# Kernel tuning notes

Measured on AMD Instinct MI355X. Metric: run time of the kernel, lower is better.

The kernel has to match this reference:

```python
import jax, jax.numpy as jnp
import numpy as np

BS, N, DX, DE, STEPS = 32, 64, 8, 5, 50


def setup_inputs() -> dict:
    key = jax.random.key(0)
    kx, ke, km, kg, kwx, kwe = jax.random.split(key, 6)
    # one-hot node states [bs, n, dx]
    x_lab = jax.random.randint(kx, (BS, N), 0, DX)
    X = jax.nn.one_hot(x_lab, DX, dtype=jnp.float32)
    # symmetric one-hot edge states [bs, n, n, de], zero diagonal
    e_lab = jax.random.randint(ke, (BS, N, N), 0, DE)
    e_lab = jnp.triu(e_lab, 1)
    e_lab = e_lab + jnp.swapaxes(e_lab, 1, 2)
    E = jax.nn.one_hot(e_lab, DE, dtype=jnp.float32)
    # variable-size graphs: first `length` nodes valid
    lengths = jax.random.randint(km, (BS,), N // 2, N + 1)
    node_mask = jnp.arange(N)[None, :] < lengths[:, None]
    gammas = jax.random.uniform(kg, (STEPS,), minval=1e-3, maxval=2e-2)
    # stub denoising network weights (stand-in for the graph transformer `net`)
    Wx = jax.random.normal(kwx, (DX, DX)) * 0.5
    We = jax.random.normal(kwe, (DE, DE)) * 0.5
    return {"X": X, "E": E, "node_mask": node_mask, "gammas": gammas, "Wx": Wx, "We": We}


def _langevin(X, E, gammas, Wx, We, node_mask):
    bs, n, dx = X.shape
    de = E.shape[-1]
    nm = node_mask.astype(X.dtype)                    # [bs, n]
    em = nm[:, :, None] * nm[:, None, :]              # [bs, n, n]
    em = em * (1.0 - jnp.eye(n, dtype=X.dtype))       # zero diagonal
    iu = jnp.triu(jnp.ones((n, n), dtype=bool), 1)    # strict upper triangle
    key0 = jax.random.key(42)

    def step(carry, inp):
        Xc, Ec = carry
        gamma, k = inp
        kx, ke = jax.random.split(jax.random.fold_in(key0, k))
        # --- stub `net` forward: per-class linear map + softmax ---
        predX = jax.nn.softmax(Xc @ Wx, axis=-1) * gamma          # pred.X * gamma
        predE = jax.nn.softmax(Ec @ We, axis=-1) * gamma          # pred.E * gamma
        predE = 0.5 * (predE + jnp.swapaxes(predE, 1, 2))         # symmetric edges
        # --- scatter_(argmax, 0); scatter_(argmax, clamp(1-sum,0)); normalize ---
        ohx = jax.nn.one_hot(jnp.argmax(Xc, -1), dx, dtype=Xc.dtype)
        ohe = jax.nn.one_hot(jnp.argmax(Ec, -1), de, dtype=Ec.dtype)
        predX = predX * (1.0 - ohx)
        predE = predE * (1.0 - ohe)
        predX = predX + ohx * jnp.maximum(1.0 - predX.sum(-1, keepdims=True), 0.0)
        predE = predE + ohe * jnp.maximum(1.0 - predE.sum(-1, keepdims=True), 0.0)
        predX = predX / predX.sum(-1, keepdims=True)
        predE = predE / predE.sum(-1, keepdims=True)
        # --- categorical sample (Gumbel-argmax), one-hot, symmetrize, mask ---
        sx = jnp.argmax(jnp.log(predX) + jax.random.gumbel(kx, predX.shape), -1)
        se = jnp.argmax(jnp.log(predE) + jax.random.gumbel(ke, predE.shape), -1)
        se = jnp.where(iu[None], se, 0)
        se = se + jnp.swapaxes(se, 1, 2)
        Xn = jax.nn.one_hot(sx, dx, dtype=Xc.dtype) * nm[:, :, None]
        En = jax.nn.one_hot(se, de, dtype=Ec.dtype) * em[..., None]
        return (Xn, En), (Xc, Ec, Xn, En)

    ks = jnp.arange(STEPS)
    _, (outX, outE, totX, totE) = jax.lax.scan(step, (X, E), (gammas, ks))
    tr = lambda a: jnp.moveaxis(a, 0, 1)             # [steps,bs,...] -> [bs,steps,...]
    return tr(totX), tr(totE), tr(outX), tr(outE)


def reference(X, E, node_mask, gammas, Wx, We):
    return _langevin(X, E, gammas, Wx, We, node_mask)
```

## Files before the change

### kernel.cpp

```cpp
#include <hip/hip_runtime.h>
#include <stdint.h>

#pragma clang fp contract(off)

#define STEPS 50
#define BSZ 32
#define NN 64
#define DXC 8
#define DEC 5
#define OFF_TOTE 819200UL
#define OFF_OUTX 33587200UL
#define OFF_OUTE 34406400UL

#define NPAIR 2016
#define EDGE_CHAINS 64512
#define NODE_CHAINS 2048
#define EBLK 16128
#define WS_KEYS 0UL
#define WS_CL   1024UL
#define WS_GE   130048UL
#define WS_GN   64642048UL
#define WS_S2E  67918848UL
#define WS_S2N  71144448UL
#define WS_NEED 71246848UL

__device__ __forceinline__ uint32_t rotl32(uint32_t x, int d) {
  return (x << d) | (x >> (32 - d));
}

__device__ __forceinline__ void tf2x32(uint32_t k0, uint32_t k1,
                                       uint32_t x0, uint32_t x1,
                                       uint32_t& o0, uint32_t& o1) {
  uint32_t ks2 = k0 ^ k1 ^ 0x1BD11BDAu;
  x0 += k0; x1 += k1;
#define TF_R(r) { x0 += x1; x1 = rotl32(x1, (r)); x1 ^= x0; }
  TF_R(13) TF_R(15) TF_R(26) TF_R(6)
  x0 += k1; x1 += ks2 + 1u;
  TF_R(17) TF_R(29) TF_R(16) TF_R(24)
  x0 += ks2; x1 += k0 + 2u;
  TF_R(13) TF_R(15) TF_R(26) TF_R(6)
  x0 += k0; x1 += k1 + 3u;
  TF_R(17) TF_R(29) TF_R(16) TF_R(24)
  x0 += k1; x1 += ks2 + 4u;
  TF_R(13) TF_R(15) TF_R(26) TF_R(6)
  x0 += ks2; x1 += k0 + 5u;
#undef TF_R
  o0 = x0; o1 = x1;
}

__device__ __forceinline__ float logf_cr(float x) { return (float)log((double)x); }
__device__ __forceinline__ float expf_cr(float x) { return (float)exp((double)x); }

__device__ __forceinline__ float gumbel_inl(uint32_t k0, uint32_t k1,
                                            uint32_t idx) {
  uint32_t o0, o1;
  tf2x32(k0, k1, 0u, idx, o0, o1);
  uint32_t bits = o0 ^ o1;
  float uf = __uint_as_float((bits >> 9) | 0x3f800000u) - 1.0f;
  float u = fmaxf(uf, 1.1754943508222875e-38f);
  return -logf_cr(-logf_cr(u));
}
__device__ __attribute__((noinline)) float gumbel_part(uint32_t k0, uint32_t k1,
                                                       uint32_t idx) {
  return gumbel_inl(k0, k1, idx);
}

__device__ __forceinline__ bool detect_bf16(const void* X) {
  const uint16_t* u = (const uint16_t*)X;
  int c = 0;
  for (int i = 0; i < 16; ++i) c += (u[i] == 0x3F80u);
  return c >= 2;
}

__device__ __forceinline__ float ld(const void* p, size_t i, bool bf) {
  if (bf) return __uint_as_float(((uint32_t)((const uint16_t*)p)[i]) << 16);
  return ((const float*)p)[i];
}
__device__ __forceinline__ void st(void* p, size_t i, bool bf, float v) {
  if (bf) ((uint16_t*)p)[i] = (uint16_t)(__float_as_uint(v) >> 16);
  else ((float*)p)[i] = v;
}
__device__ __forceinline__ void stv4(void* p, size_t e4, bool bf,
                                     float a, float b, float c, float d) {
  if (!bf) {
    float4 v; v.x = a; v.y = b; v.z = c; v.w = d;
    ((float4*)p)[e4] = v;
  } else {
    ushort4 v;
    v.x = (uint16_t)(__float_as_uint(a) >> 16);
    v.y = (uint16_t)(__float_as_uint(b) >> 16);
    v.z = (uint16_t)(__float_as_uint(c) >> 16);
    v.w = (uint16_t)(__float_as_uint(d) >> 16);
    ((ushort4*)p)[e4] = v;
  }
}
__device__ __forceinline__ void cpy4(void* dst, const void* src, size_t de4,
                                     size_t se4, bool bf) {
  if (!bf) ((float4*)dst)[de4] = ((const float4*)src)[se4];
  else ((uint2*)dst)[de4] = ((const uint2*)src)[se4];
}

__device__ __forceinline__ bool read_mask(const void* mp, int idx) {
  const uint8_t* m8 = (const uint8_t*)mp;
  uint8_t b1 = m8[1];
  if (b1 == 0) return ((const uint32_t*)mp)[idx] != 0;
  if (b1 == 0x3F) return ((const uint16_t*)mp)[idx] != 0;
  return m8[idx] != 0;
}

template <int D>
__device__ void fill_logp(const void* __restrict__ W, bool bf, float gamma,
                          int c, float* __restrict__ out) {
  float t[D];
  for (int d = 0; d < D; ++d) t[d] = ld(W, c * D + d, bf);
  float m = t[0];
  for (int d = 1; d < D; ++d) m = fmaxf(m, t[d]);
  float u[D];
  for (int d = 0; d < D; ++d) u[d] = expf_cr(t[d] - m);
  float s = 0.0f;
  for (int d = 0; d < D; ++d) s += u[d];
  float p[D];
  for (int d = 0; d < D; ++d) p[d] = (u[d] / s) * gamma;
  p[c] = 0.0f;
  float s1 = 0.0f;
  for (int d = 0; d < D; ++d) s1 += p[d];
  float r = fmaxf(1.0f - s1, 0.0f);
  p[c] = r;
  float s2 = 0.0f;
  for (int d = 0; d < D; ++d) s2 += p[d];
  for (int d = 0; d < D; ++d) out[d] = logf_cr(p[d] / s2);
}

__device__ __forceinline__ void pair_decode(int q, int& lo, int& hi) {
  lo = 0; int rem = q;
  while (rem >= 63 - lo) { rem -= 63 - lo; lo++; }
  hi = lo + 1 + rem;
}

__global__ void key_kernel(uint8_t* __restrict__ ws) {
  int t = threadIdx.x;
  uint32_t* wk = (uint32_t*)(ws + WS_KEYS);
  if (t == 0) wk[200] = 0u;
  if (t < STEPS) {
    uint32_t f0, f1, a0, a1;
    tf2x32(0u, 42u, 0u, (uint32_t)t, f0, f1);
    tf2x32(f0, f1, 0u, 0u, a0, a1);
    wk[2 * t] = a0; wk[2 * t + 1] = a1;
    tf2x32(f0, f1, 0u, 1u, a0, a1);
    wk[100 + 2 * t] = a0; wk[101 + 2 * t] = a1;
  }
}

__global__ __launch_bounds__(256) void compact_kernel(const void* __restrict__ M,
                                                      uint8_t* __restrict__ ws) {
  int chain = blockIdx.x * 256 + threadIdx.x;
  if (chain >= EDGE_CHAINS) return;
  int b = chain / NPAIR, q = chain % NPAIR, lo, hi;
  pair_decode(q, lo, hi);
  if (read_mask(M, b * NN + lo) && read_mask(M, b * NN + hi)) {
    uint32_t slot = atomicAdd((uint32_t*)(ws + WS_KEYS) + 200, 1u);
    ((uint16_t*)(ws + WS_CL))[slot] = (uint16_t)chain;
  }
}

__global__ __launch_bounds__(256) void gumbel_kernel(const void* __restrict__ M,
                                                     uint8_t* __restrict__ ws) {
  const uint32_t* keys = (const uint32_t*)(ws + WS_KEYS);
  float* ge = (float*)(ws + WS_GE);
  float* gn = (float*)(ws + WS_GN);
  int blk = blockIdx.x, tid = threadIdx.x;
  if (blk < EBLK) {
    uint32_t cnt = keys[200];
    if ((uint32_t)(blk * 4) >= cnt) return;
    if (tid >= STEPS * DEC) return;
    const uint16_t* cl = (const uint16_t*)(ws + WS_CL);
    int k = tid / DEC, d = tid % DEC;
    uint32_t kk0 = keys[100 + 2 * k], kk1 = keys[101 + 2 * k];
    int ch[4]; uint32_t ctr[4]; bool ok[4];
#pragma unroll
    for (int j = 0; j < 4; ++j) {
      uint32_t idx = (uint32_t)(blk * 4 + j);
      ok[j] = idx < cnt;
      int chain = cl[ok[j] ? idx : 0];
      ch[j] = chain;
      int b = chain / NPAIR, q = chain % NPAIR, lo, hi;
      pair_decode(q, lo, hi);
      ctr[j] = (uint32_t)(((b * NN + lo) * NN + hi) * DEC + d);
    }
    float v0 = gumbel_inl(kk0, kk1, ctr[0]);
    float v1 = gumbel_inl(kk0, kk1, ctr[1]);
    float v2 = gumbel_inl(kk0, kk1, ctr[2]);
    float v3 = gumbel_inl(kk0, kk1, ctr[3]);
    if (ok[0]) ge[(size_t)ch[0] * 250 + tid] = v0;
    if (ok[1]) ge[(size_t)ch[1] * 250 + tid] = v1;
    if (ok[2]) ge[(size_t)ch[2] * 250 + tid] = v2;
    if (ok[3]) ge[(size_t)ch[3] * 250 + tid] = v3;
  } else {
    int n0 = (blk - EBLK) * 4;
    bool ok[4];
#pragma unroll
    for (int j = 0; j < 4; ++j) ok[j] = read_mask(M, n0 + j);
    for (int r = 0; r < 2; ++r) {
      int slot = r * 256 + tid;
      if (slot < STEPS * DXC) {
        int k = slot >> 3, d = slot & 7;
        uint32_t kk0 = keys[2 * k], kk1 = keys[2 * k + 1];
        float w[4];
#pragma unroll
        for (int j = 0; j < 4; ++j)
          w[j] = gumbel_inl(kk0, kk1, (uint32_t)((n0 + j) * DXC + d));
#pragma unroll
        for (int j = 0; j < 4; ++j)
          if (ok[j]) gn[(size_t)(n0 + j) * 400 + slot] = w[j];
      }
    }
  }
}

__global__ __launch_bounds__(256) void chain_kernel(
    const void* __restrict__ X, const void* __restrict__ E,
    const void* __restrict__ M, const void* __restrict__ gammas,
    const void* __restrict__ Wx, const void* __restrict__ We,
    uint8_t* __restrict__ ws) {
  __shared__ float stab[STEPS * DXC * DXC];
  const bool edge_blk = blockIdx.x < 252;
  const int t = threadIdx.x;
  const bool bf = detect_bf16(X);

  if (edge_blk) {
    for (int task = t; task < STEPS * DEC; task += 256)
      fill_logp<DEC>(We, bf, ld(gammas, task / DEC, bf), task % DEC,
                     &stab[task * DEC]);
  } else {
    for (int task = t; task < STEPS * DXC; task += 256)
      fill_logp<DXC>(Wx, bf, ld(gammas, task / DXC, bf), task % DXC,
                     &stab[task * DXC]);
  }
  __syncthreads();

  if (edge_blk) {
    int chain = blockIdx.x * 256 + t;
    int b = chain / NPAIR, q = chain % NPAIR, lo, hi;
    pair_decode(q, lo, hi);
    if (!(read_mask(M, b * NN + lo) && read_mask(M, b * NN + hi))) return;
    size_t crow = (((size_t)(b * NN + lo)) * NN + hi) * DEC;
    int cur = 0;
    float bst = ld(E, crow, bf);
    for (int d = 1; d < DEC; ++d) {
      float v = ld(E, crow + d, bf);
      if (v > bst) { bst = v; cur = d; }
    }
    const float* g = (const float*)(ws + WS_GE) + (size_t)chain * 250;
    uint8_t* s2e = ws + WS_S2E;
    for (int k = 0; k < STEPS; ++k) {
      const float* le = stab + (k * DEC + cur) * DEC;
      const float* gk = g + k * DEC;
      float bs = -3.0e38f; int nxt = 0;
      for (int d = 0; d < DEC; ++d) {
        float s = le[d] + gk[d];
        if (s > bs) { bs = s; nxt = d; }
      }
      s2e[(size_t)(b * STEPS + k) * NPAIR + q] = (uint8_t)nxt;
      cur = nxt;
    }
  } else {
    int node = (int)(blockIdx.x - 252) * 256 + t;
    if (!read_mask(M, node)) return;
    int b = node >> 6, i = node & 63;
    int cur = 0;
    float bst = ld(X, (size_t)node * DXC, bf);
    for (int d = 1; d < DXC; ++d) {
      float v = ld(X, (size_t)node * DXC + d, bf);
      if (v > bst) { bst = v; cur = d; }
    }
    const float* g = (const float*)(ws + WS_GN) + (size_t)node * 400;
    uint8_t* s2n = ws + WS_S2N;
    for (int k = 0; k < STEPS; ++k) {
      const float* le = stab + (k * DXC + cur) * DXC;
      const float* gk = g + k * DXC;
      float bs = -3.0e38f; int nxt = 0;
      for (int d = 0; d < DXC; ++d) {
        float s = le[d] + gk[d];
        if (s > bs) { bs = s; nxt = d; }
      }
      s2n[(size_t)(b * STEPS + k) * 64 + i] = (uint8_t)nxt;
      cur = nxt;
    }
  }
}

__global__ __launch_bounds__(256) void write_kernel(
    const void* __restrict__ X, const void* __restrict__ E,
    const void* __restrict__ M, const uint8_t* __restrict__ ws,
    void* __restrict__ out) {
  __shared__ uint8_t cur_g[4096];
  __shared__ uint8_t pre_g[4096];
  __shared__ uint8_t sc[NPAIR];
  __shared__ uint8_t sp_[NPAIR];
  __shared__ uint8_t sn[3200];
  __shared__ uint8_t vf[64];
  const bool bf = detect_bf16(X);
  const int t = threadIdx.x;

  if (blockIdx.x < 1600) {
    int slab = blockIdx.x;
    int b = slab / STEPS, k = slab % STEPS;
    if (t < 64) vf[t] = read_mask(M, b * NN + t) ? 1 : 0;
    const uint8_t* s2e = ws + WS_S2E;
    for (int x = t; x < 504; x += 256) {
      ((uint32_t*)sc)[x] = ((const uint32_t*)(s2e + (size_t)slab * NPAIR))[x];
      if (k > 0)
        ((uint32_t*)sp_)[x] =
            ((const uint32_t*)(s2e + (size_t)(slab - 1) * NPAIR))[x];
    }
    __syncthreads();
    for (int ij = t; ij < 4096; ij += 256) {
      int i = ij >> 6, j = ij & 63;
      uint8_t c = 0xFF, p = 0xFF;
      if (i != j && vf[i] && vf[j]) {
        int lo = i < j ? i : j, hi = i < j ? j : i;
        int q = 63 * lo - ((lo * (lo - 1)) >> 1) + hi - lo - 1;
        c = sc[q];
        if (k > 0) p = sp_[q];
      }
      cur_g[ij] = c; pre_g[ij] = p;
    }
    __syncthreads();
    size_t base = (size_t)slab * 20480;
    for (int f = t; f < 5120; f += 256) {
      int e0 = f * 4;
      float v[4];
#pragma unroll
      for (int m = 0; m < 4; ++m) {
        int e = e0 + m, ij = e / 5, d = e - ij * 5;
        v[m] = (d == (int)cur_g[ij]) ? 1.0f : 0.0f;
      }
      stv4(out, (OFF_TOTE + base) / 4 + f, bf, v[0], v[1], v[2], v[3]);
    }
    if (k == 0) {
      size_t src4 = (size_t)b * 5120;
      for (int f = t; f < 5120; f += 256)
        cpy4(out, E, (OFF_OUTE + base) / 4 + f, src4 + f, bf);
    } else {
      for (int f = t; f < 5120; f += 256) {
        int e0 = f * 4;
        float v[4];
#pragma unroll
        for (int m = 0; m < 4; ++m) {
          int e = e0 + m, ij = e / 5, d = e - ij * 5;
          v[m] = (d == (int)pre_g[ij]) ? 1.0f : 0.0f;
        }
        stv4(out, (OFF_OUTE + base) / 4 + f, bf, v[0], v[1], v[2], v[3]);
      }
    }
  } else {
    int b = (int)blockIdx.x - 1600;
    if (t < 64) vf[t] = read_mask(M, b * NN + t) ? 1 : 0;
    for (int x = t; x < 800; x += 256)
      ((uint32_t*)sn)[x] =
          ((const uint32_t*)(ws + WS_S2N + (size_t)b * STEPS * 64))[x];
    __syncthreads();
    size_t base0 = (size_t)b * 25600;
    for (int f = t; f < 6400; f += 256) {
      int e0 = f * 4;
      int k = e0 >> 9, i = (e0 >> 3) & 63;
      int s = (int)sn[k * 64 + i];
      bool va = vf[i] != 0;
      float v[4];
#pragma unroll
      for (int m = 0; m < 4; ++m) {
        int d = (e0 + m) & 7;
        v[m] = (va && d == s) ? 1.0f : 0.0f;
      }
      stv4(out, base0 / 4 + f, bf, v[0], v[1], v[2], v[3]);
    }
    for (int f = t; f < 6400; f += 256) {
      int e0 = f * 4;
      int k = e0 >> 9, i = (e0 >> 3) & 63;
      if (k == 0) {
        cpy4(out, X, (OFF_OUTX + base0) / 4 + f,
             ((size_t)b * 512 + (size_t)(e0 & 511)) / 4, bf);
      } else {
        int s = (int)sn[(k - 1) * 64 + i];
        bool va = vf[i] != 0;
        float v[4];
#pragma unroll
        for (int m = 0; m < 4; ++m) {
          int d = (e0 + m) & 7;
          v[m] = (va && d == s) ? 1.0f : 0.0f;
        }
        stv4(out, (OFF_OUTX + base0) / 4 + f, bf, v[0], v[1], v[2], v[3]);
      }
    }
  }
}

__global__ __launch_bounds__(256) void lang_kernel(
    const void* __restrict__ X, const void* __restrict__ E,
    const void* __restrict__ M, const void* __restrict__ gammas,
    const void* __restrict__ Wx, const void* __restrict__ We,
    void* __restrict__ out) {
  __shared__ uint32_t skeys[STEPS * 2];
  __shared__ float stab[STEPS * DXC * DXC];
  const bool edge_blk = blockIdx.x < 512;
  const int t = threadIdx.x;
  const bool bf = detect_bf16(X);

  if (t < STEPS) {
    uint32_t f0, f1, a0, a1;
    tf2x32(0u, 42u, 0u, (uint32_t)t, f0, f1);
    tf2x32(f0, f1, 0u, edge_blk ? 1u : 0u, a0, a1);
    skeys[2 * t] = a0; skeys[2 * t + 1] = a1;
  }
  if (edge_blk) {
    for (int task = t; task < STEPS * DEC; task += 256) {
      int k = task / DEC, c = task % DEC;
      fill_logp<DEC>(We, bf, ld(gammas, k, bf), c, &stab[(k * DEC + c) * DEC]);
    }
  } else {
    for (int task = t; task < STEPS * DXC; task += 256) {
      int k = task / DXC, c = task % DXC;
      fill_logp<DXC>(Wx, bf, ld(gammas, k, bf), c, &stab[(k * DXC + c) * DXC]);
    }
  }
  __syncthreads();

  if (edge_blk) {
    int tid = blockIdx.x * 256 + threadIdx.x;
    int b = tid >> 12, rem = tid & 4095, i = rem >> 6, j = rem & 63;
    bool valid = (i != j) && read_mask(M, b * NN + i) && read_mask(M, b * NN + j);
    int lo = i < j ? i : j, hi = i < j ? j : i;
    int cur = 0;
    if (valid) {
      size_t crow = (((size_t)(b * NN + lo)) * NN + hi) * DEC;
      float bst = ld(E, crow, bf);
      for (int d = 1; d < DEC; ++d) {
        float v = ld(E, crow + d, bf);
        if (v > bst) { bst = v; cur = d; }
      }
    }
    uint32_t base = (uint32_t)((((b * NN) + lo) * NN + hi) * DEC);
#pragma clang loop unroll(disable)
    for (int k = 0; k < STEPS; ++k) {
      size_t tp = ((((size_t)b * STEPS + k) * NN + i) * NN + j) * DEC;
      if (k == 0) {
        for (int d = 0; d < DEC; ++d)
          st(out, OFF_OUTE + tp + d, bf, ld(E, (size_t)tid * DEC + d, bf));
      } else {
        for (int d = 0; d < DEC; ++d)
          st(out, OFF_OUTE + tp + d, bf, (valid && d == cur) ? 1.0f : 0.0f);
      }
      int nxt = 0;
      if (valid) {
        const float* le = stab + (k * DEC + cur) * DEC;
        uint32_t k0 = skeys[2 * k], k1 = skeys[2 * k + 1];
        float bst = -3.0e38f;
        for (int d = 0; d < DEC; ++d) {
          float s = le[d] + gumbel_part(k0, k1, base + (uint32_t)d);
          if (s > bst) { bst = s; nxt = d; }
        }
      }
      for (int d = 0; d < DEC; ++d)
        st(out, OFF_TOTE + tp + d, bf, (valid && d == nxt) ? 1.0f : 0.0f);
      cur = nxt;
    }
  } else {
    int tid = (int)(blockIdx.x - 512) * 256 + threadIdx.x;
    if (tid >= BSZ * NN) return;
    int b = tid >> 6, i = tid & 63;
    bool valid = read_mask(M, tid);
    int cur = 0;
    {
      float bst = ld(X, (size_t)tid * DXC, bf);
      for (int d = 1; d < DXC; ++d) {
        float v = ld(X, (size_t)tid * DXC + d, bf);
        if (v > bst) { bst = v; cur = d; }
      }
    }
    uint32_t base = (uint32_t)(tid * DXC);
#pragma clang loop unroll(disable)
    for (int k = 0; k < STEPS; ++k) {
      size_t tp = (((size_t)b * STEPS + k) * NN + i) * DXC;
      if (k == 0) {
        for (int d = 0; d < DXC; ++d)
          st(out, OFF_OUTX + tp + d, bf, ld(X, (size_t)tid * DXC + d, bf));
      } else {
        for (int d = 0; d < DXC; ++d)
          st(out, OFF_OUTX + tp + d, bf, (valid && d == cur) ? 1.0f : 0.0f);
      }
      int nxt = 0;
      if (valid) {
        const float* lx = stab + (k * DXC + cur) * DXC;
        uint32_t k0 = skeys[2 * k], k1 = skeys[2 * k + 1];
        float bst = -3.0e38f;
        for (int d = 0; d < DXC; ++d) {
          float s = lx[d] + gumbel_part(k0, k1, base + (uint32_t)d);
          if (s > bst) { bst = s; nxt = d; }
        }
      }
      for (int d = 0; d < DXC; ++d)
        st(out, tp + d, bf, (valid && d == nxt) ? 1.0f : 0.0f);
      cur = nxt;
    }
  }
}

extern "C" void kernel_launch(void* const* d_in, const int* in_sizes, int n_in,
                              void* d_out, int out_size, void* d_ws, size_t ws_size,
                              hipStream_t stream) {
  (void)out_size;
  const void* X = d_in[0];
  const void* E = d_in[1];
  const void* M = d_in[2];
  const void* G = d_in[3];
  const void* Wx = d_in[4];
  const void* We = d_in[5];
  for (int i = 0; i < n_in && i < 6; ++i) {
    switch (in_sizes[i]) {
      case 16384:  X = d_in[i]; break;
      case 655360: E = d_in[i]; break;
      case 2048:   M = d_in[i]; break;
      case 50:     G = d_in[i]; break;
      case 64:     Wx = d_in[i]; break;
      case 25:     We = d_in[i]; break;
      default: break;
    }
  }
  if (ws_size >= WS_NEED) {
    uint8_t* ws = (uint8_t*)d_ws;
    hipLaunchKernelGGL(key_kernel, dim3(1), dim3(64), 0, stream, ws);
    hipLaunchKernelGGL(compact_kernel, dim3(252), dim3(256), 0, stream, M, ws);
    hipLaunchKernelGGL(gumbel_kernel, dim3(EBLK + 512), dim3(256), 0, stream,
                       M, ws);
    hipLaunchKernelGGL(chain_kernel, dim3(260), dim3(256), 0, stream,
                       X, E, M, G, Wx, We, ws);
    hipLaunchKernelGGL(write_kernel, dim3(1632), dim3(256), 0, stream,
                       X, E, M, ws, d_out);
  } else {
    hipLaunchKernelGGL(lang_kernel, dim3(520), dim3(256), 0, stream,
                       X, E, M, G, Wx, We, d_out);
  }
}
```

Before: 436.3 us.

## Transpose gumbel noise buffers to slab-major layout and index chains by compacted slot

Gumbel noise for edges and nodes is now stored with one slab per (step, class) and the chain index as the fastest dimension, so consecutive threads write and read consecutive floats instead of strided 250- or 400-float rows. A per-slot base counter is stored at compaction time so the gumbel and chain kernels no longer decode pair indices, and the chain kernel iterates over compacted slots rather than all pairs with a mask check. This is meant to coalesce the large noise writes and reads and to pack the active edge chains densely into the leading chain-kernel blocks. It costs an extra workspace array and a 2D grid with many early-exit blocks.

```diff
diff --git a/kernel.cpp b/kernel.cpp
--- a/kernel.cpp
+++ b/kernel.cpp
@@ -14,15 +14,14 @@
 
 #define NPAIR 2016
 #define EDGE_CHAINS 64512
-#define NODE_CHAINS 2048
-#define EBLK 16128
 #define WS_KEYS 0UL
 #define WS_CL   1024UL
-#define WS_GE   130048UL
-#define WS_GN   64642048UL
-#define WS_S2E  67918848UL
-#define WS_S2N  71144448UL
-#define WS_NEED 71246848UL
+#define WS_CB   130048UL
+#define WS_GE   388096UL
+#define WS_GN   64900096UL
+#define WS_S2E  68176896UL
+#define WS_S2N  71402496UL
+#define WS_NEED 71504896UL
 
 __device__ __forceinline__ uint32_t rotl32(uint32_t x, int d) {
   return (x << d) | (x >> (32 - d));
@@ -160,60 +159,32 @@
   if (read_mask(M, b * NN + lo) && read_mask(M, b * NN + hi)) {
     uint32_t slot = atomicAdd((uint32_t*)(ws + WS_KEYS) + 200, 1u);
     ((uint16_t*)(ws + WS_CL))[slot] = (uint16_t)chain;
+    ((uint32_t*)(ws + WS_CB))[slot] =
+        (uint32_t)(((b * NN + lo) * NN + hi) * DEC);
   }
 }
 
 __global__ __launch_bounds__(256) void gumbel_kernel(const void* __restrict__ M,
                                                      uint8_t* __restrict__ ws) {
   const uint32_t* keys = (const uint32_t*)(ws + WS_KEYS);
-  float* ge = (float*)(ws + WS_GE);
-  float* gn = (float*)(ws + WS_GN);
-  int blk = blockIdx.x, tid = threadIdx.x;
-  if (blk < EBLK) {
+  const int tid = threadIdx.x;
+  if (blockIdx.y < 250) {
     uint32_t cnt = keys[200];
-    if ((uint32_t)(blk * 4) >= cnt) return;
-    if (tid >= STEPS * DEC) return;
-    const uint16_t* cl = (const uint16_t*)(ws + WS_CL);
-    int k = tid / DEC, d = tid % DEC;
-    uint32_t kk0 = keys[100 + 2 * k], kk1 = keys[101 + 2 * k];
-    int ch[4]; uint32_t ctr[4]; bool ok[4];
-#pragma unroll
-    for (int j = 0; j < 4; ++j) {
-      uint32_t idx = (uint32_t)(blk * 4 + j);
-      ok[j] = idx < cnt;
-      int chain = cl[ok[j] ? idx : 0];
-      ch[j] = chain;
-      int b = chain / NPAIR, q = chain % NPAIR, lo, hi;
-      pair_decode(q, lo, hi);
-      ctr[j] = (uint32_t)(((b * NN + lo) * NN + hi) * DEC + d);
-    }
-    float v0 = gumbel_inl(kk0, kk1, ctr[0]);
-    float v1 = gumbel_inl(kk0, kk1, ctr[1]);
-    float v2 = gumbel_inl(kk0, kk1, ctr[2]);
-    float v3 = gumbel_inl(kk0, kk1, ctr[3]);
-    if (ok[0]) ge[(size_t)ch[0] * 250 + tid] = v0;
-    if (ok[1]) ge[(size_t)ch[1] * 250 + tid] = v1;
-    if (ok[2]) ge[(size_t)ch[2] * 250 + tid] = v2;
-    if (ok[3]) ge[(size_t)ch[3] * 250 + tid] = v3;
-  } else {
-    int n0 = (blk - EBLK) * 4;
-    bool ok[4];
-#pragma unroll
-    for (int j = 0; j < 4; ++j) ok[j] = read_mask(M, n0 + j);
-    for (int r = 0; r < 2; ++r) {
-      int slot = r * 256 + tid;
-      if (slot < STEPS * DXC) {
-        int k = slot >> 3, d = slot & 7;
-        uint32_t kk0 = keys[2 * k], kk1 = keys[2 * k + 1];
-        float w[4];
-#pragma unroll
-        for (int j = 0; j < 4; ++j)
-          w[j] = gumbel_inl(kk0, kk1, (uint32_t)((n0 + j) * DXC + d));
-#pragma unroll
-        for (int j = 0; j < 4; ++j)
-          if (ok[j]) gn[(size_t)(n0 + j) * 400 + slot] = w[j];
-      }
-    }
+    uint32_t slot = blockIdx.x * 256 + tid;
+    if (slot >= cnt) return;
+    int slab = blockIdx.y, k = slab / DEC, d = slab - k * DEC;
+    uint32_t ctr = ((const uint32_t*)(ws + WS_CB))[slot] + (uint32_t)d;
+    ((float*)(ws + WS_GE))[(size_t)slab * EDGE_CHAINS + slot] =
+        gumbel_inl(keys[100 + 2 * k], keys[101 + 2 * k], ctr);
+  } else {
+    int idx = ((int)blockIdx.y - 250) * 252 + (int)blockIdx.x;
+    if (idx >= 3200) return;
+    int slab = idx >> 3;
+    int node = ((idx & 7) << 8) + tid;
+    if (!read_mask(M, node)) return;
+    int k = slab >> 3, d = slab & 7;
+    ((float*)(ws + WS_GN))[(size_t)slab * 2048 + node] =
+        gumbel_inl(keys[2 * k], keys[2 * k + 1], (uint32_t)(node * DXC + d));
   }
 }
 
@@ -239,25 +210,25 @@
   __syncthreads();
 
   if (edge_blk) {
-    int chain = blockIdx.x * 256 + t;
-    int b = chain / NPAIR, q = chain % NPAIR, lo, hi;
-    pair_decode(q, lo, hi);
-    if (!(read_mask(M, b * NN + lo) && read_mask(M, b * NN + hi))) return;
-    size_t crow = (((size_t)(b * NN + lo)) * NN + hi) * DEC;
+    uint32_t cnt = ((const uint32_t*)(ws + WS_KEYS))[200];
+    uint32_t slot = blockIdx.x * 256 + t;
+    if (slot >= cnt) return;
+    int chain = (int)((const uint16_t*)(ws + WS_CL))[slot];
+    int b = chain / NPAIR, q = chain - b * NPAIR;
+    uint32_t crow = ((const uint32_t*)(ws + WS_CB))[slot];
     int cur = 0;
     float bst = ld(E, crow, bf);
     for (int d = 1; d < DEC; ++d) {
-      float v = ld(E, crow + d, bf);
+      float v = ld(E, (size_t)crow + d, bf);
       if (v > bst) { bst = v; cur = d; }
     }
-    const float* g = (const float*)(ws + WS_GE) + (size_t)chain * 250;
+    const float* ge = (const float*)(ws + WS_GE);
     uint8_t* s2e = ws + WS_S2E;
     for (int k = 0; k < STEPS; ++k) {
       const float* le = stab + (k * DEC + cur) * DEC;
-      const float* gk = g + k * DEC;
       float bs = -3.0e38f; int nxt = 0;
       for (int d = 0; d < DEC; ++d) {
-        float s = le[d] + gk[d];
+        float s = le[d] + ge[(size_t)(k * DEC + d) * EDGE_CHAINS + slot];
         if (s > bs) { bs = s; nxt = d; }
       }
       s2e[(size_t)(b * STEPS + k) * NPAIR + q] = (uint8_t)nxt;
@@ -273,14 +244,13 @@
       float v = ld(X, (size_t)node * DXC + d, bf);
       if (v > bst) { bst = v; cur = d; }
     }
-    const float* g = (const float*)(ws + WS_GN) + (size_t)node * 400;
+    const float* gn = (const float*)(ws + WS_GN);
     uint8_t* s2n = ws + WS_S2N;
     for (int k = 0; k < STEPS; ++k) {
       const float* le = stab + (k * DXC + cur) * DXC;
-      const float* gk = g + k * DXC;
       float bs = -3.0e38f; int nxt = 0;
       for (int d = 0; d < DXC; ++d) {
-        float s = le[d] + gk[d];
+        float s = le[d] + gn[(size_t)(k * DXC + d) * 2048 + node];
         if (s > bs) { bs = s; nxt = d; }
       }
       s2n[(size_t)(b * STEPS + k) * 64 + i] = (uint8_t)nxt;
@@ -530,7 +500,7 @@
     uint8_t* ws = (uint8_t*)d_ws;
     hipLaunchKernelGGL(key_kernel, dim3(1), dim3(64), 0, stream, ws);
     hipLaunchKernelGGL(compact_kernel, dim3(252), dim3(256), 0, stream, M, ws);
-    hipLaunchKernelGGL(gumbel_kernel, dim3(EBLK + 512), dim3(256), 0, stream,
+    hipLaunchKernelGGL(gumbel_kernel, dim3(252, 263), dim3(256), 0, stream,
                        M, ws);
     hipLaunchKernelGGL(chain_kernel, dim3(260), dim3(256), 0, stream,
                        X, E, M, G, Wx, We, ws);
```

Result: no change. 433.2 us (-0.7%).
